# Optimization experiments

Measured on AMD Instinct MI355X. Metric: run time of the kernel, lower is better.

Reference implementation:

```python
import jax, jax.numpy as jnp
import numpy as np

HIDDEN = 16  # hidden_channels; conv outputs 3*HIDDEN gate channels

def setup_inputs() -> dict:
    key = jax.random.key(0)
    k1, k2 = jax.random.split(key)
    inputs = jax.random.normal(k1, (4, 16, 31, 128, 128), dtype=jnp.float32)
    # Conv3d weight (O, I, D, H, W); scaled down so tanh/sigmoid gates are not saturated
    W = jax.random.normal(k2, (3 * HIDDEN, 16, 3, 3, 3), dtype=jnp.float32) * 0.05
    b = jnp.zeros((3 * HIDDEN,), dtype=jnp.float32)
    return {"inputs": inputs, "W": W, "b": b}

def reference(inputs, W, b):
    # conv step: Conv3d with padding=1 (SAME for kernel 3, stride 1)
    gates = jax.lax.conv_general_dilated(
        inputs, W, window_strides=(1, 1, 1), padding='SAME',
        dimension_numbers=('NCDHW', 'OIDHW', 'NCDHW'))
    gates = gates + b[None, :, None, None, None]
    Z, F, O = jnp.split(gates, 3, axis=1)
    Z = jnp.tanh(Z)
    F = jax.nn.sigmoid(F)
    O = jax.nn.sigmoid(O)
    # fo-pooling: sequential linear recurrence over time axis (dim 2)
    Zt = jnp.moveaxis(Z, 2, 0)  # (T, N, C, H, W)
    Ft = jnp.moveaxis(F, 2, 0)
    Ot = jnp.moveaxis(O, 2, 0)
    c0 = jnp.zeros_like(Zt[0])  # c=None at t=0 is equivalent to c0=0

    def step(c, zfo):
        z, f, o = zfo
        c = f * c + (1.0 - f) * z
        return c, o * c

    _, h = jax.lax.scan(step, c0, (Zt, Ft, Ot))
    return jnp.moveaxis(h, 0, 2)  # back to (N, C, T, H, W)
```

## Files before the change

kernel.cpp:

```cpp
#include <hip/hip_runtime.h>


typedef __attribute__((ext_vector_type(8))) short short8;
typedef __attribute__((ext_vector_type(4))) float float4v;

#define TD 31
#define HW (128 * 128)
#define LH 6
#define LW 34
#define UNITS (LH * 2 * LW)
#define NSLOT 3
#define WUNITS (14 * 3 * 64)

__device__ __forceinline__ short f2bf(float f) {
    unsigned u = __float_as_uint(f);
    u = (u + 0x7FFFu + ((u >> 16) & 1u)) >> 16;
    return (short)u;
}

__global__ __launch_bounds__(256, 2) void qrnn_mfma2(
    const float* __restrict__ x,
    const float* __restrict__ wt,
    const float* __restrict__ bias,
    float* __restrict__ out)
{
    __shared__ short8 wlds[WUNITS];
    __shared__ short8 ring[NSLOT * UNITS];

    const int tid  = threadIdx.x;
    const int lane = tid & 63;
    const int wv   = tid >> 6;
    const int q    = lane >> 4;
    const int px   = lane & 15;
    const int b    = blockIdx.x;
    const int n    = b >> 7;
    const int h0   = ((b >> 2) & 31) * 4;
    const int w0   = (b & 3) * 32;

    const float* xin = x + (size_t)n * (16 * TD * HW);

    for (int k = 0; k < 11; ++k) {
        int u = tid + k * 256;
        if (u < WUNITS) {
            int l = u & 63, rest = u >> 6;
            int g = rest % 3, s = rest / 3;
            int qq = l >> 4, m = l & 15;
            short8 a;
#pragma unroll
            for (int j = 0; j < 8; ++j) {
                int kk = s * 32 + qq * 8 + j;
                int tap = kk >> 4, ic = kk & 15;
                float v = (tap < 27) ? wt[((size_t)((g * 16 + m) * 16 + ic)) * 27 + tap] : 0.f;
                a[j] = f2bf(v);
            }
            wlds[u] = a;
        }
    }

    float rv[2][8];
    int s_hp[2], s_wp[2], s_ck[2]; bool s_in[2];
#pragma unroll
    for (int i = 0; i < 2; ++i) {
        int u  = tid + i * 256;
        int uu = (u < UNITS) ? u : 0;
        s_wp[i] = uu % LW;
        int rest = uu / LW;
        s_ck[i] = rest & 1;
        s_hp[i] = rest >> 1;
        s_in[i] = (u < UNITS);
    }

    auto issue_loads = [&](int tt) {
        const bool tz = ((unsigned)tt >= 31u);
        const int tc = tz ? 0 : tt;
#pragma unroll
        for (int i = 0; i < 2; ++i) {
            int hh = h0 + s_hp[i] - 1;
            int ww = w0 + s_wp[i] - 1;
            bool ok = s_in[i] && !tz && ((unsigned)hh < 128u) && ((unsigned)ww < 128u);
            const float* src = xin + ((size_t)(s_ck[i] * 8) * TD + tc) * HW + hh * 128 + ww;
#pragma unroll
            for (int j = 0; j < 8; ++j)
                rv[i][j] = ok ? src[(size_t)j * TD * HW] : 0.f;
        }
    };
    auto write_lds = [&](int slot) {
#pragma unroll
        for (int i = 0; i < 2; ++i) {
            if (s_in[i]) {
                short8 v;
#pragma unroll
                for (int j = 0; j < 8; ++j) v[j] = f2bf(rv[i][j]);
                ring[slot * UNITS + tid + i * 256] = v;
            }
        }
    };

    float bval[3][4];
#pragma unroll
    for (int g = 0; g < 3; ++g)
#pragma unroll
        for (int r = 0; r < 4; ++r)
            bval[g][r] = bias[g * 16 + q * 4 + r];

    float* po = out + ((size_t)(n * 16 + q * 4) * TD) * HW
                    + (size_t)(h0 + wv) * 128 + w0 + px;
    float cst[2][4] = {{0.f,0.f,0.f,0.f},{0.f,0.f,0.f,0.f}};

    issue_loads(-1); write_lds(0);
    issue_loads(0);  write_lds(1);
    issue_loads(1);  write_lds(2);
    __syncthreads();

    for (int t = 0; t < TD; ++t) {
        const int t3 = t % 3;
        issue_loads(t + 2);

        float4v acc[2][3];
#pragma unroll
        for (int g = 0; g < 3; ++g) {
            float4v bv = (float4v){bval[g][0], bval[g][1], bval[g][2], bval[g][3]};
            acc[0][g] = bv; acc[1][g] = bv;
        }

#pragma unroll
        for (int s = 0; s < 14; ++s) {
            int T = 2 * s + (q >> 1); if (T > 26) T = 26;
            int kd = T / 9, rr = T - kd * 9, kh = rr / 3, kw = rr - kh * 3;
            int slot = t3 + kd; if (slot >= NSLOT) slot -= NSLOT;
            int base = slot * UNITS + ((wv + kh) * 2 + (q & 1)) * LW + px + kw;
            short8 b0 = ring[base];
            short8 b1 = ring[base + 16];
#pragma unroll
            for (int g = 0; g < 3; ++g) {
                short8 wf = wlds[(s * 3 + g) * 64 + lane];
                acc[0][g] = __builtin_amdgcn_mfma_f32_16x16x32_bf16(wf, b0, acc[0][g], 0, 0, 0);
                acc[1][g] = __builtin_amdgcn_mfma_f32_16x16x32_bf16(wf, b1, acc[1][g], 0, 0, 0);
            }
        }
        __syncthreads();
        write_lds(t3);

#pragma unroll
        for (int tile = 0; tile < 2; ++tile) {
#pragma unroll
            for (int r = 0; r < 4; ++r) {
                float az = acc[tile][0][r];
                float af = acc[tile][1][r];
                float ao = acc[tile][2][r];
                float z = 1.f - 2.f / (__expf(2.f * az) + 1.f);
                float f = 1.f / (1.f + __expf(-af));
                float o = 1.f / (1.f + __expf(-ao));
                float c = f * cst[tile][r] + (1.f - f) * z;
                cst[tile][r] = c;
                po[(size_t)r * (TD * HW) + tile * 16] = o * c;
            }
        }
        po += HW;
        __syncthreads();
    }
}

extern "C" void kernel_launch(void* const* d_in, const int* in_sizes, int n_in,
                              void* d_out, int out_size, void* d_ws, size_t ws_size,
                              hipStream_t stream) {
    const float* x    = (const float*)d_in[0];
    const float* wt   = (const float*)d_in[1];
    const float* bias = (const float*)d_in[2];
    float* out = (float*)d_out;

    qrnn_mfma2<<<dim3(512), dim3(256), 0, stream>>>(x, wt, bias, out);
}
```

Baseline: 305.6 us.

## Deepen input prefetch to two timesteps with ping-pong registers and precomputed offsets

Global loads for the input halo are now issued three timesteps ahead into alternating register buffers (rvA/rvB), with the loop unrolled by two, so loads have a full extra step of MFMA work to hide latency. Per-element addresses and LDS ring offsets are precomputed once, and ring slot bases rotate in registers, which removes index arithmetic from the inner loop. Barriers become a raw lgkmcnt wait plus s_barrier so outstanding global loads are not drained, and divisions in the gate activations use hardware reciprocal. This costs more registers, which could threaten two-block occupancy, and the fast rcp trades a little accuracy.

```diff
diff --git a/kernel.cpp b/kernel.cpp
--- a/kernel.cpp
+++ b/kernel.cpp
@@ -10,6 +10,7 @@
 #define LW 34
 #define UNITS (LH * 2 * LW)
 #define NSLOT 3
+#define SLOTB (UNITS * 16)
 #define WUNITS (14 * 3 * 64)
 
 __device__ __forceinline__ short f2bf(float f) {
@@ -18,7 +19,11 @@
     return (short)u;
 }
 
-__global__ __launch_bounds__(256, 2) void qrnn_mfma2(
+__device__ __forceinline__ float frcp(float x) { return __builtin_amdgcn_rcpf(x); }
+
+#define BARRIER() asm volatile("s_waitcnt lgkmcnt(0)\n\ts_barrier" ::: "memory")
+
+__global__ __launch_bounds__(256, 2) void qrnn_mfma3(
     const float* __restrict__ x,
     const float* __restrict__ wt,
     const float* __restrict__ bias,
@@ -57,80 +62,98 @@
         }
     }
 
-    float rv[2][8];
-    int s_hp[2], s_wp[2], s_ck[2]; bool s_in[2];
+    int  s_off[2][8];
+    bool s_in[2], s_ok[2];
 #pragma unroll
     for (int i = 0; i < 2; ++i) {
-        int u  = tid + i * 256;
-        int uu = (u < UNITS) ? u : 0;
-        s_wp[i] = uu % LW;
+        int u    = tid + i * 256;
+        int uu   = (u < UNITS) ? u : 0;
+        int wp   = uu % LW;
         int rest = uu / LW;
-        s_ck[i] = rest & 1;
-        s_hp[i] = rest >> 1;
+        int ck   = rest & 1;
+        int hp   = rest >> 1;
+        int hh   = h0 + hp - 1;
+        int ww   = w0 + wp - 1;
         s_in[i] = (u < UNITS);
-    }
-
-    auto issue_loads = [&](int tt) {
+        s_ok[i] = s_in[i] && ((unsigned)hh < 128u) && ((unsigned)ww < 128u);
+        int hc = hh < 0 ? 0 : (hh > 127 ? 127 : hh);
+        int wc = ww < 0 ? 0 : (ww > 127 ? 127 : ww);
+#pragma unroll
+        for (int j = 0; j < 8; ++j)
+            s_off[i][j] = ((ck * 8 + j) * TD) * HW + hc * 128 + wc;
+    }
+
+    float rvA[2][8], rvB[2][8];
+
+    auto issue = [&](int tt, float (&rv)[2][8]) {
         const bool tz = ((unsigned)tt >= 31u);
-        const int tc = tz ? 0 : tt;
+        const int  tc = tz ? 0 : tt;
+        const float* basep = xin + (size_t)tc * HW;
 #pragma unroll
         for (int i = 0; i < 2; ++i) {
-            int hh = h0 + s_hp[i] - 1;
-            int ww = w0 + s_wp[i] - 1;
-            bool ok = s_in[i] && !tz && ((unsigned)hh < 128u) && ((unsigned)ww < 128u);
-            const float* src = xin + ((size_t)(s_ck[i] * 8) * TD + tc) * HW + hh * 128 + ww;
-#pragma unroll
-            for (int j = 0; j < 8; ++j)
-                rv[i][j] = ok ? src[(size_t)j * TD * HW] : 0.f;
+            bool ok = s_ok[i] && !tz;
+#pragma unroll
+            for (int j = 0; j < 8; ++j) {
+                float v = basep[s_off[i][j]];
+                rv[i][j] = ok ? v : 0.f;
+            }
         }
     };
-    auto write_lds = [&](int slot) {
+
+    auto lds_write = [&](int wu, float (&rv)[2][8]) {
 #pragma unroll
         for (int i = 0; i < 2; ++i) {
             if (s_in[i]) {
                 short8 v;
 #pragma unroll
                 for (int j = 0; j < 8; ++j) v[j] = f2bf(rv[i][j]);
-                ring[slot * UNITS + tid + i * 256] = v;
+                ring[wu + tid + i * 256] = v;
             }
         }
     };
 
-    float bval[3][4];
+    int roff[14];
+#pragma unroll
+    for (int s = 0; s < 14; ++s) {
+        int T = 2 * s + (q >> 1); if (T > 26) T = 26;
+        int kd = T / 9, rr = T - kd * 9, kh = rr / 3, kw = rr - kh * 3;
+        roff[s] = (((wv + kh) * 2 + (q & 1)) * LW + px + kw) * 16;
+    }
+    const int kd4 = q >> 1;
+
+    float4v bv[3];
 #pragma unroll
     for (int g = 0; g < 3; ++g)
-#pragma unroll
-        for (int r = 0; r < 4; ++r)
-            bval[g][r] = bias[g * 16 + q * 4 + r];
+        bv[g] = (float4v){bias[g * 16 + q * 4 + 0], bias[g * 16 + q * 4 + 1],
+                          bias[g * 16 + q * 4 + 2], bias[g * 16 + q * 4 + 3]};
 
     float* po = out + ((size_t)(n * 16 + q * 4) * TD) * HW
                     + (size_t)(h0 + wv) * 128 + w0 + px;
     float cst[2][4] = {{0.f,0.f,0.f,0.f},{0.f,0.f,0.f,0.f}};
 
-    issue_loads(-1); write_lds(0);
-    issue_loads(0);  write_lds(1);
-    issue_loads(1);  write_lds(2);
-    __syncthreads();
-
-    for (int t = 0; t < TD; ++t) {
-        const int t3 = t % 3;
-        issue_loads(t + 2);
+    issue(-1, rvA); lds_write(0,         rvA);
+    issue(0,  rvA); lds_write(UNITS,     rvA);
+    issue(1,  rvA); lds_write(2 * UNITS, rvA);
+    issue(2,  rvA);
+    BARRIER();
+
+    auto body = [&](int t, int pk0, int pk1, int pk2, int wu,
+                    float (&rvW)[2][8], float (&rvI)[2][8]) {
+        issue(t + 3, rvI);
 
         float4v acc[2][3];
 #pragma unroll
-        for (int g = 0; g < 3; ++g) {
-            float4v bv = (float4v){bval[g][0], bval[g][1], bval[g][2], bval[g][3]};
-            acc[0][g] = bv; acc[1][g] = bv;
-        }
-
+        for (int g = 0; g < 3; ++g) { acc[0][g] = bv[g]; acc[1][g] = bv[g]; }
+
+        const int pk[3] = {pk0, pk1, pk2};
+        constexpr int kdt[14] = {0,0,0,0, 0 , 1,1,1,1, 2,2,2,2,2};
+        const char* ringb = (const char*)ring;
 #pragma unroll
         for (int s = 0; s < 14; ++s) {
-            int T = 2 * s + (q >> 1); if (T > 26) T = 26;
-            int kd = T / 9, rr = T - kd * 9, kh = rr / 3, kw = rr - kh * 3;
-            int slot = t3 + kd; if (slot >= NSLOT) slot -= NSLOT;
-            int base = slot * UNITS + ((wv + kh) * 2 + (q & 1)) * LW + px + kw;
-            short8 b0 = ring[base];
-            short8 b1 = ring[base + 16];
+            int sb = (s == 4) ? (kd4 ? pk1 : pk0) : pk[kdt[s]];
+            const short8* bp = (const short8*)(ringb + sb + roff[s]);
+            short8 b0 = bp[0];
+            short8 b1 = bp[16];
 #pragma unroll
             for (int g = 0; g < 3; ++g) {
                 short8 wf = wlds[(s * 3 + g) * 64 + lane];
@@ -138,8 +161,8 @@
                 acc[1][g] = __builtin_amdgcn_mfma_f32_16x16x32_bf16(wf, b1, acc[1][g], 0, 0, 0);
             }
         }
-        __syncthreads();
-        write_lds(t3);
+        BARRIER();
+        lds_write(wu, rvW);
 
 #pragma unroll
         for (int tile = 0; tile < 2; ++tile) {
@@ -148,17 +171,28 @@
                 float az = acc[tile][0][r];
                 float af = acc[tile][1][r];
                 float ao = acc[tile][2][r];
-                float z = 1.f - 2.f / (__expf(2.f * az) + 1.f);
-                float f = 1.f / (1.f + __expf(-af));
-                float o = 1.f / (1.f + __expf(-ao));
+                float z = 1.f - 2.f * frcp(__expf(2.f * az) + 1.f);
+                float f = frcp(1.f + __expf(-af));
+                float o = frcp(1.f + __expf(-ao));
                 float c = f * cst[tile][r] + (1.f - f) * z;
                 cst[tile][r] = c;
                 po[(size_t)r * (TD * HW) + tile * 16] = o * c;
             }
         }
         po += HW;
-        __syncthreads();
-    }
+        BARRIER();
+    };
+
+    int pk0 = 0, pk1 = SLOTB, pk2 = 2 * SLOTB;
+    int wu = 0;
+    for (int t = 0; t < 30; t += 2) {
+        body(t,     pk0, pk1, pk2, wu,  rvA, rvB);
+        int wu1 = (wu == 2 * UNITS) ? 0 : wu + UNITS;
+        body(t + 1, pk1, pk2, pk0, wu1, rvB, rvA);
+        int t0 = pk0; pk0 = pk2; pk2 = pk1; pk1 = t0;
+        wu = (wu1 == 2 * UNITS) ? 0 : wu1 + UNITS;
+    }
+    body(30, pk0, pk1, pk2, wu, rvA, rvB);
 }
 
 extern "C" void kernel_launch(void* const* d_in, const int* in_sizes, int n_in,
@@ -169,5 +203,5 @@
     const float* bias = (const float*)d_in[2];
     float* out = (float*)d_out;
 
-    qrnn_mfma2<<<dim3(512), dim3(256), 0, stream>>>(x, wt, bias, out);
+    qrnn_mfma3<<<dim3(512), dim3(256), 0, stream>>>(x, wt, bias, out);
 }
```

New measurement: 292.1 us. 1.05x faster.
